# Kernel optimization log

Measured on AMD Instinct MI355X. Metric: run time of the kernel, lower is better.

The kernel has to match this reference:

```python
import jax, jax.numpy as jnp
import numpy as np

N = 4096      # (num_domains+1) * batch_size
F_IN = 512    # nfeat
HID = 64      # nhid per head
H = 8         # nheads
ALPHA = 0.2   # leaky-relu negative slope
EDGE_P = 0.01 # adjacency density


def setup_inputs() -> dict:
    key = jax.random.key(0)
    k1, k2, k3, k4 = jax.random.split(key, 4)
    x = jax.random.normal(k1, (N, F_IN), dtype=jnp.float32)
    adj = (jax.random.uniform(k2, (N, N)) < EDGE_P).astype(jnp.float32)
    # ensure self-loops so every row has at least one valid edge for softmax
    adj = jnp.maximum(adj, jnp.eye(N, dtype=jnp.float32))
    W = jax.random.normal(k3, (H, F_IN, HID), dtype=jnp.float32) * 0.1
    a = jax.random.normal(k4, (H, 2 * HID), dtype=jnp.float32) * 0.1
    return {"x": x, "adj": adj, "W": W, "a": a}


def reference(x, adj, W, a):
    # Wh: [H, N, HID] -- per-head linear projection
    Wh = jnp.einsum('nf,hfd->hnd', x, W)
    # additive attention logits: e_ij = leakyrelu(a1.Wh_i + a2.Wh_j)
    e_src = jnp.einsum('hnd,hd->hn', Wh, a[:, :HID])   # [H, N]
    e_dst = jnp.einsum('hnd,hd->hn', Wh, a[:, HID:])   # [H, N]
    e = jax.nn.leaky_relu(e_src[:, :, None] + e_dst[:, None, :], ALPHA)  # [H, N, N]
    e = jnp.where(adj[None] > 0, e, jnp.float32(-9e15))
    att = jax.nn.softmax(e, axis=-1)                    # masked softmax over neighbors
    h = jnp.einsum('hnm,hmd->hnd', att, Wh)             # [H, N, HID]
    h = jax.nn.elu(h)                                   # concat=True -> elu per head
    # concat heads: [N, H*HID]
    return jnp.transpose(h, (1, 0, 2)).reshape(N, H * HID)
```

## Files before the change

kernel.cpp:

```cpp
#include <hip/hip_runtime.h>
#include <hip/hip_bf16.h>
#include <math.h>

#define N_NODES 4096
#define F_IN    512
#define HID     64
#define H       8
#define NJ      512
#define ALPHA   0.2f

typedef __bf16 bf16x8 __attribute__((ext_vector_type(8)));
typedef float  f32x4  __attribute__((ext_vector_type(4)));

#define A_CHUNKS (N_NODES * F_IN / 8)
#define B_CHUNKS (NJ * F_IN / 8)

__global__ __launch_bounds__(256) void conv_prep(const float* __restrict__ x,
                                                 const float* __restrict__ W,
                                                 __bf16* __restrict__ AhT,
                                                 __bf16* __restrict__ AlT,
                                                 __bf16* __restrict__ BthT) {
    int id = blockIdx.x * 256 + threadIdx.x;
    if (id < A_CHUNKS) {
        int u  = id & 511;
        int kt = (id >> 9) & 7;
        int bm = id >> 12;
        int r  = u >> 3, c8 = u & 7;
        int col = kt * 64 + ((c8 ^ (r & 7)) << 3);
        const float4* gp = (const float4*)(x + (size_t)(bm * 64 + r) * F_IN + col);
        float4 v0 = gp[0];
        float4 v1 = gp[1];
        float vv[8] = {v0.x, v0.y, v0.z, v0.w, v1.x, v1.y, v1.z, v1.w};
        bf16x8 hv, lv;
        #pragma unroll
        for (int e = 0; e < 8; e++) {
            __bf16 hi = (__bf16)vv[e];
            hv[e] = hi;
            lv[e] = (__bf16)(vv[e] - (float)hi);
        }
        *(bf16x8*)(AhT + (size_t)id * 8) = hv;
        *(bf16x8*)(AlT + (size_t)id * 8) = lv;
    } else {
        int bid = id - A_CHUNKS;
        if (bid < B_CHUNKS) {
            int u  = bid & 511;
            int kt = (bid >> 9) & 7;
            int h  = bid >> 12;
            int r  = u >> 3, c8 = u & 7;
            int kb = kt * 64 + ((c8 ^ (r & 7)) << 3);
            bf16x8 hv;
            #pragma unroll
            for (int e = 0; e < 8; e++) {
                hv[e] = (__bf16)W[((size_t)h * F_IN + kb + e) * HID + r];
            }
            *(bf16x8*)(BthT + (size_t)bid * 8) = hv;
        }
    }
}

__device__ __forceinline__ void async16(void* lds, const void* g) {
    __builtin_amdgcn_global_load_lds(
        (const __attribute__((address_space(1))) unsigned int*)g,
        (__attribute__((address_space(3))) unsigned int*)lds, 16, 0, 0);
}

__global__ __launch_bounds__(256) void wh_gemm(const __bf16* __restrict__ AhT,
                                               const __bf16* __restrict__ AlT,
                                               const __bf16* __restrict__ BthT,
                                               const float* __restrict__ a,
                                               __bf16* __restrict__ Whb,
                                               float* __restrict__ esrc,
                                               float* __restrict__ edst) {
    const int bid = blockIdx.x;
    const int xcd = bid & 7;
    const int s0  = bid >> 3;
    const int bm  = xcd * 8 + (s0 >> 3);
    const int h   = s0 & 7;

    const int tid  = threadIdx.x;
    const int wave = tid >> 6;
    const int lane = tid & 63;
    const int lm = lane & 15;
    const int lq = lane >> 4;

    __shared__ __align__(16) __bf16 smem[3 * 4096];
    __bf16* Ash = smem;
    __bf16* Asl = smem + 4096;
    __bf16* Bsh = smem + 8192;

    f32x4 acc[4];
    #pragma unroll
    for (int c = 0; c < 4; c++) acc[c] = (f32x4){0.f, 0.f, 0.f, 0.f};

    const __bf16* tA_h = AhT  + (size_t)bm * (8 * 4096);
    const __bf16* tA_l = AlT  + (size_t)bm * (8 * 4096);
    const __bf16* tB   = BthT + (size_t)h  * (8 * 4096);

    const int rowA = wave * 16 + lm;

    for (int kt = 0; kt < 8; kt++) {
        const size_t ko = (size_t)kt * 4096;
        #pragma unroll
        for (int s = 0; s < 2; s++) {
            int u  = s * 256 + tid;
            int ub = s * 256 + wave * 64;
            async16(Ash + ub * 8, tA_h + ko + (size_t)u * 8);
            async16(Asl + ub * 8, tA_l + ko + (size_t)u * 8);
            async16(Bsh + ub * 8, tB   + ko + (size_t)u * 8);
        }
        __syncthreads();

        #pragma unroll
        for (int kh = 0; kh < 2; kh++) {
            const int ce = (((kh << 2) + lq) ^ (lm & 7)) << 3;
            bf16x8 afh = *(const bf16x8*)&Ash[rowA * 64 + ce];
            bf16x8 afl = *(const bf16x8*)&Asl[rowA * 64 + ce];
            bf16x8 bh[4];
            #pragma unroll
            for (int c = 0; c < 4; c++) {
                bh[c] = *(const bf16x8*)&Bsh[(c * 16 + lm) * 64 + ce];
            }
            #pragma unroll
            for (int c = 0; c < 4; c++) {
                acc[c] = __builtin_amdgcn_mfma_f32_16x16x32_bf16(afh, bh[c], acc[c], 0, 0, 0);
                acc[c] = __builtin_amdgcn_mfma_f32_16x16x32_bf16(afl, bh[c], acc[c], 0, 0, 0);
            }
        }
        __syncthreads();
    }

    float a1c[4], a2c[4];
    #pragma unroll
    for (int c = 0; c < 4; c++) {
        a1c[c] = a[h * 2 * HID + c * 16 + lm];
        a2c[c] = a[h * 2 * HID + HID + c * 16 + lm];
    }

    #pragma unroll
    for (int r = 0; r < 4; r++) {
        int row = bm * 64 + wave * 16 + lq * 4 + r;
        float s1 = 0.f, s2 = 0.f;
        #pragma unroll
        for (int c = 0; c < 4; c++) {
            float v = acc[c][r];
            Whb[(size_t)row * NJ + h * HID + c * 16 + lm] = (__bf16)v;
            s1 += v * a1c[c];
            s2 += v * a2c[c];
        }
        #pragma unroll
        for (int o = 1; o < 16; o <<= 1) {
            s1 += __shfl_xor(s1, o);
            s2 += __shfl_xor(s2, o);
        }
        if (lm == 0) {
            esrc[h * N_NODES + row] = s1;
            edst[h * N_NODES + row] = s2;
        }
    }
}

#define MAXN 128

__global__ __launch_bounds__(256) void gat_attn(const float* __restrict__ adj,
                                                const __bf16* __restrict__ Whb,
                                                const float* __restrict__ esrc,
                                                const float* __restrict__ edst,
                                                float* __restrict__ out) {
    const int i    = blockIdx.x;
    const int tid  = threadIdx.x;
    const int wave = tid >> 6;
    const int lane = tid & 63;
    __shared__ int    nbr[MAXN];
    __shared__ __align__(8)  float2 an[H][MAXN + 4];
    __shared__ float  denom[H];
    __shared__ __align__(16) f32x4 part[3][2][64];
    __shared__ int    cnt;

    if (tid == 0) cnt = 0;
    __syncthreads();

    const unsigned long long lt = (1ull << lane) - 1ull;
    const f32x4* arow = (const f32x4*)(adj + (size_t)i * N_NODES);
    f32x4 q[4];
    #pragma unroll
    for (int cc = 0; cc < 4; cc++) q[cc] = __builtin_nontemporal_load(arow + cc * 256 + tid);
    #pragma unroll
    for (int cc = 0; cc < 4; cc++) {
        unsigned long long b0 = __ballot(q[cc][0] > 0.f);
        unsigned long long b1 = __ballot(q[cc][1] > 0.f);
        unsigned long long b2 = __ballot(q[cc][2] > 0.f);
        unsigned long long b3 = __ballot(q[cc][3] > 0.f);
        int c0 = __popcll(b0), c1 = __popcll(b1), c2 = __popcll(b2), c3 = __popcll(b3);
        int base = 0;
        if (lane == 0) base = atomicAdd(&cnt, c0 + c1 + c2 + c3);
        base = __shfl(base, 0);
        int col = (cc * 256 + tid) * 4;
        if (q[cc][0] > 0.f) nbr[base + __popcll(b0 & lt)] = col;
        base += c0;
        if (q[cc][1] > 0.f) nbr[base + __popcll(b1 & lt)] = col + 1;
        base += c1;
        if (q[cc][2] > 0.f) nbr[base + __popcll(b2 & lt)] = col + 2;
        base += c2;
        if (q[cc][3] > 0.f) nbr[base + __popcll(b3 & lt)] = col + 3;
    }
    __syncthreads();
    const int n = cnt;

    #pragma unroll
    for (int k = 0; k < 2; k++) {
        const int hh = wave * 2 + k;
        float es = esrc[hh * N_NODES + i];
        float m = -1e30f;
        for (int j = lane; j < n; j += 64) {
            int c = nbr[j];
            float lg = es + edst[hh * N_NODES + c];
            lg = lg > 0.f ? lg : ALPHA * lg;
            an[hh][j] = make_float2(lg, __int_as_float(c << 10));
            m = fmaxf(m, lg);
        }
        #pragma unroll
        for (int o = 32; o; o >>= 1) m = fmaxf(m, __shfl_xor(m, o));
        float s = 0.f;
        for (int j = lane; j < n; j += 64) {
            float w = __expf(an[hh][j].x - m);
            an[hh][j].x = w;
            s += w;
        }
        #pragma unroll
        for (int o = 32; o; o >>= 1) s += __shfl_xor(s, o);
        if (lane == 0) denom[hh] = s;
    }
    __syncthreads();

    const int qd = tid >> 6;
    const int t  = tid & 63;
    const int h  = t >> 3;
    const char* wp = (const char*)Whb + t * 16;
    float a0 = 0.f, a1 = 0.f, a2 = 0.f, a3 = 0.f;
    float a4 = 0.f, a5 = 0.f, a6 = 0.f, a7 = 0.f;
    #pragma unroll 4
    for (int j = qd; j < n; j += 4) {
        float2 p = an[h][j];
        uint4 u = *(const uint4*)(wp + __float_as_uint(p.y));
        float w = p.x;
        a0 += w * __uint_as_float(u.x << 16);
        a1 += w * __uint_as_float(u.x & 0xffff0000u);
        a2 += w * __uint_as_float(u.y << 16);
        a3 += w * __uint_as_float(u.y & 0xffff0000u);
        a4 += w * __uint_as_float(u.z << 16);
        a5 += w * __uint_as_float(u.z & 0xffff0000u);
        a6 += w * __uint_as_float(u.w << 16);
        a7 += w * __uint_as_float(u.w & 0xffff0000u);
    }
    if (qd) {
        part[qd - 1][0][t] = (f32x4){a0, a1, a2, a3};
        part[qd - 1][1][t] = (f32x4){a4, a5, a6, a7};
    }
    __syncthreads();
    if (qd == 0) {
        f32x4 r0 = (f32x4){a0, a1, a2, a3};
        f32x4 r1 = (f32x4){a4, a5, a6, a7};
        #pragma unroll
        for (int s = 0; s < 3; s++) {
            r0 += part[s][0][t];
            r1 += part[s][1][t];
        }
        float inv = 1.f / denom[h];
        float b[8];
        #pragma unroll
        for (int e = 0; e < 4; e++) b[e] = r0[e] * inv;
        #pragma unroll
        for (int e = 0; e < 4; e++) b[4 + e] = r1[e] * inv;
        #pragma unroll
        for (int e = 0; e < 8; e++) b[e] = b[e] > 0.f ? b[e] : expm1f(b[e]);
        f32x4 o0 = (f32x4){b[0], b[1], b[2], b[3]};
        f32x4 o1 = (f32x4){b[4], b[5], b[6], b[7]};
        f32x4* op = (f32x4*)(out + (size_t)i * NJ + t * 8);
        __builtin_nontemporal_store(o0, op);
        __builtin_nontemporal_store(o1, op + 1);
    }
}

extern "C" void kernel_launch(void* const* d_in, const int* in_sizes, int n_in,
                              void* d_out, int out_size, void* d_ws, size_t ws_size,
                              hipStream_t stream) {
    const float* x   = (const float*)d_in[0];
    const float* adj = (const float*)d_in[1];
    const float* W   = (const float*)d_in[2];
    const float* a   = (const float*)d_in[3];
    float* out = (float*)d_out;

    float*  esrc = (float*)d_ws;
    float*  edst = esrc + (size_t)H * N_NODES;
    __bf16* Whb  = (__bf16*)(edst + (size_t)H * N_NODES);
    __bf16* AhT  = Whb + (size_t)N_NODES * NJ;
    __bf16* AlT  = AhT + (size_t)N_NODES * F_IN;
    __bf16* BthT = AlT + (size_t)N_NODES * F_IN;

    conv_prep<<<(A_CHUNKS + B_CHUNKS) / 256, 256, 0, stream>>>(x, W, AhT, AlT, BthT);

    wh_gemm<<<512, 256, 0, stream>>>(AhT, AlT, BthT, a, Whb, esrc, edst);

    gat_attn<<<N_NODES, 256, 0, stream>>>(adj, Whb, esrc, edst, out);
}
```

Before: 135.8 us.

## Double-buffer projection GEMM loads and rebalance attention gather lanes

The projection GEMM now double-buffers its LDS tiles. The next k-tile is issued with async loads before computing the current one, using vmcnt waits and raw s_barrier in place of full syncthreads. In the attention kernel, the neighbor-weighted gather now uses 128 threads per half, each handling 4 features with 8-byte loads, instead of 64 threads x 4 quarters with 16-byte loads. This halves the cross-wave reduction but gives each thread twice as many iterations. Nontemporal loads and stores on the adjacency and output are replaced with ordinary accesses. The GEMM's LDS footprint doubles, which may lower occupancy.

```diff
diff --git a/kernel.cpp b/kernel.cpp
--- a/kernel.cpp
+++ b/kernel.cpp
@@ -83,10 +83,7 @@
     const int lm = lane & 15;
     const int lq = lane >> 4;
 
-    __shared__ __align__(16) __bf16 smem[3 * 4096];
-    __bf16* Ash = smem;
-    __bf16* Asl = smem + 4096;
-    __bf16* Bsh = smem + 8192;
+    __shared__ __align__(16) __bf16 smem[2 * 3 * 4096];
 
     f32x4 acc[4];
     #pragma unroll
@@ -98,17 +95,35 @@
 
     const int rowA = wave * 16 + lm;
 
-    for (int kt = 0; kt < 8; kt++) {
-        const size_t ko = (size_t)kt * 4096;
+    auto stage = [&](int buf, int kt2) {
+        __bf16* base = smem + buf * 12288;
+        const size_t ko = (size_t)kt2 * 4096;
         #pragma unroll
         for (int s = 0; s < 2; s++) {
             int u  = s * 256 + tid;
             int ub = s * 256 + wave * 64;
-            async16(Ash + ub * 8, tA_h + ko + (size_t)u * 8);
-            async16(Asl + ub * 8, tA_l + ko + (size_t)u * 8);
-            async16(Bsh + ub * 8, tB   + ko + (size_t)u * 8);
-        }
-        __syncthreads();
+            async16(base +        ub * 8, tA_h + ko + (size_t)u * 8);
+            async16(base + 4096 + ub * 8, tA_l + ko + (size_t)u * 8);
+            async16(base + 8192 + ub * 8, tB   + ko + (size_t)u * 8);
+        }
+    };
+
+    stage(0, 0);
+
+    for (int kt = 0; kt < 8; kt++) {
+        const int cur = kt & 1;
+        if (kt < 7) {
+            stage(1 - cur, kt + 1);
+            asm volatile("s_waitcnt vmcnt(6)" ::: "memory");
+        } else {
+            asm volatile("s_waitcnt vmcnt(0)" ::: "memory");
+        }
+        __builtin_amdgcn_s_barrier();
+        __builtin_amdgcn_sched_barrier(0);
+
+        const __bf16* Ash = smem + cur * 12288;
+        const __bf16* Asl = Ash + 4096;
+        const __bf16* Bsh = Ash + 8192;
 
         #pragma unroll
         for (int kh = 0; kh < 2; kh++) {
@@ -126,7 +141,7 @@
                 acc[c] = __builtin_amdgcn_mfma_f32_16x16x32_bf16(afl, bh[c], acc[c], 0, 0, 0);
             }
         }
-        __syncthreads();
+        __builtin_amdgcn_s_barrier();
     }
 
     float a1c[4], a2c[4];
@@ -171,113 +186,94 @@
     const int wave = tid >> 6;
     const int lane = tid & 63;
     __shared__ int    nbr[MAXN];
-    __shared__ __align__(8)  float2 an[H][MAXN + 4];
+    __shared__ __align__(8)  float2 an[H][MAXN];
     __shared__ float  denom[H];
-    __shared__ __align__(16) f32x4 part[3][2][64];
+    __shared__ __align__(16) float4 part[128];
     __shared__ int    cnt;
 
     if (tid == 0) cnt = 0;
     __syncthreads();
 
     const unsigned long long lt = (1ull << lane) - 1ull;
-    const f32x4* arow = (const f32x4*)(adj + (size_t)i * N_NODES);
-    f32x4 q[4];
-    #pragma unroll
-    for (int cc = 0; cc < 4; cc++) q[cc] = __builtin_nontemporal_load(arow + cc * 256 + tid);
+    const float4* arow = (const float4*)(adj + (size_t)i * N_NODES);
+    float4 q[4];
+    #pragma unroll
+    for (int cc = 0; cc < 4; cc++) q[cc] = arow[cc * 256 + tid];
     #pragma unroll
     for (int cc = 0; cc < 4; cc++) {
-        unsigned long long b0 = __ballot(q[cc][0] > 0.f);
-        unsigned long long b1 = __ballot(q[cc][1] > 0.f);
-        unsigned long long b2 = __ballot(q[cc][2] > 0.f);
-        unsigned long long b3 = __ballot(q[cc][3] > 0.f);
+        unsigned long long b0 = __ballot(q[cc].x > 0.f);
+        unsigned long long b1 = __ballot(q[cc].y > 0.f);
+        unsigned long long b2 = __ballot(q[cc].z > 0.f);
+        unsigned long long b3 = __ballot(q[cc].w > 0.f);
         int c0 = __popcll(b0), c1 = __popcll(b1), c2 = __popcll(b2), c3 = __popcll(b3);
         int base = 0;
         if (lane == 0) base = atomicAdd(&cnt, c0 + c1 + c2 + c3);
         base = __shfl(base, 0);
         int col = (cc * 256 + tid) * 4;
-        if (q[cc][0] > 0.f) nbr[base + __popcll(b0 & lt)] = col;
+        if (q[cc].x > 0.f) nbr[base + __popcll(b0 & lt)] = col;
         base += c0;
-        if (q[cc][1] > 0.f) nbr[base + __popcll(b1 & lt)] = col + 1;
+        if (q[cc].y > 0.f) nbr[base + __popcll(b1 & lt)] = col + 1;
         base += c1;
-        if (q[cc][2] > 0.f) nbr[base + __popcll(b2 & lt)] = col + 2;
+        if (q[cc].z > 0.f) nbr[base + __popcll(b2 & lt)] = col + 2;
         base += c2;
-        if (q[cc][3] > 0.f) nbr[base + __popcll(b3 & lt)] = col + 3;
+        if (q[cc].w > 0.f) nbr[base + __popcll(b3 & lt)] = col + 3;
     }
     __syncthreads();
     const int n = cnt;
 
     #pragma unroll
     for (int k = 0; k < 2; k++) {
-        const int hh = wave * 2 + k;
-        float es = esrc[hh * N_NODES + i];
+        const int h = wave * 2 + k;
+        float es = esrc[h * N_NODES + i];
         float m = -1e30f;
         for (int j = lane; j < n; j += 64) {
             int c = nbr[j];
-            float lg = es + edst[hh * N_NODES + c];
+            float lg = es + edst[h * N_NODES + c];
             lg = lg > 0.f ? lg : ALPHA * lg;
-            an[hh][j] = make_float2(lg, __int_as_float(c << 10));
+            an[h][j] = make_float2(lg, __int_as_float(c << 10));
             m = fmaxf(m, lg);
         }
         #pragma unroll
         for (int o = 32; o; o >>= 1) m = fmaxf(m, __shfl_xor(m, o));
         float s = 0.f;
         for (int j = lane; j < n; j += 64) {
-            float w = __expf(an[hh][j].x - m);
-            an[hh][j].x = w;
+            float w = __expf(an[h][j].x - m);
+            an[h][j].x = w;
             s += w;
         }
         #pragma unroll
         for (int o = 32; o; o >>= 1) s += __shfl_xor(s, o);
-        if (lane == 0) denom[hh] = s;
+        if (lane == 0) denom[h] = s;
     }
     __syncthreads();
 
-    const int qd = tid >> 6;
-    const int t  = tid & 63;
-    const int h  = t >> 3;
-    const char* wp = (const char*)Whb + t * 16;
+    const int qd = tid >> 7;
+    const int t  = tid & 127;
+    const int h  = t >> 4;
+    const char* wp = (const char*)Whb + t * 8;
     float a0 = 0.f, a1 = 0.f, a2 = 0.f, a3 = 0.f;
-    float a4 = 0.f, a5 = 0.f, a6 = 0.f, a7 = 0.f;
     #pragma unroll 4
-    for (int j = qd; j < n; j += 4) {
+    for (int j = qd; j < n; j += 2) {
         float2 p = an[h][j];
-        uint4 u = *(const uint4*)(wp + __float_as_uint(p.y));
+        uint2 u = *(const uint2*)(wp + __float_as_uint(p.y));
         float w = p.x;
         a0 += w * __uint_as_float(u.x << 16);
         a1 += w * __uint_as_float(u.x & 0xffff0000u);
         a2 += w * __uint_as_float(u.y << 16);
         a3 += w * __uint_as_float(u.y & 0xffff0000u);
-        a4 += w * __uint_as_float(u.z << 16);
-        a5 += w * __uint_as_float(u.z & 0xffff0000u);
-        a6 += w * __uint_as_float(u.w << 16);
-        a7 += w * __uint_as_float(u.w & 0xffff0000u);
-    }
-    if (qd) {
-        part[qd - 1][0][t] = (f32x4){a0, a1, a2, a3};
-        part[qd - 1][1][t] = (f32x4){a4, a5, a6, a7};
-    }
+    }
+    if (qd) part[t] = make_float4(a0, a1, a2, a3);
     __syncthreads();
     if (qd == 0) {
-        f32x4 r0 = (f32x4){a0, a1, a2, a3};
-        f32x4 r1 = (f32x4){a4, a5, a6, a7};
-        #pragma unroll
-        for (int s = 0; s < 3; s++) {
-            r0 += part[s][0][t];
-            r1 += part[s][1][t];
-        }
+        float4 p = part[t];
+        a0 += p.x; a1 += p.y; a2 += p.z; a3 += p.w;
         float inv = 1.f / denom[h];
-        float b[8];
-        #pragma unroll
-        for (int e = 0; e < 4; e++) b[e] = r0[e] * inv;
-        #pragma unroll
-        for (int e = 0; e < 4; e++) b[4 + e] = r1[e] * inv;
-        #pragma unroll
-        for (int e = 0; e < 8; e++) b[e] = b[e] > 0.f ? b[e] : expm1f(b[e]);
-        f32x4 o0 = (f32x4){b[0], b[1], b[2], b[3]};
-        f32x4 o1 = (f32x4){b[4], b[5], b[6], b[7]};
-        f32x4* op = (f32x4*)(out + (size_t)i * NJ + t * 8);
-        __builtin_nontemporal_store(o0, op);
-        __builtin_nontemporal_store(o1, op + 1);
+        a0 *= inv; a1 *= inv; a2 *= inv; a3 *= inv;
+        a0 = a0 > 0.f ? a0 : expm1f(a0);
+        a1 = a1 > 0.f ? a1 : expm1f(a1);
+        a2 = a2 > 0.f ? a2 : expm1f(a2);
+        a3 = a3 > 0.f ? a3 : expm1f(a3);
+        *(float4*)(out + (size_t)i * NJ + t * 4) = make_float4(a0, a1, a2, a3);
     }
 }
 
```

New measurement: 130.0 us, median of 2. -4.2%, faster.
